# Kernel optimization log

Hardware: AMD Instinct MI355X
Metric: run time of the kernel (lower is better)

The kernel has to match this reference:

```python
import jax, jax.numpy as jnp
import numpy as np

B, N, P, D = 256, 196, 768, 768
FIXED_MASK = 40          # FIXED_MASK_COUNT in the TF source
FIXED_UNMASK = N - FIXED_MASK


def setup_inputs() -> dict:
    key = jax.random.key(0)
    k1, k2, k3, k4, k5 = jax.random.split(key, 5)
    return {
        "patches": jax.random.normal(k1, (B, N, P), jnp.float32),
        "rand_u": jax.random.uniform(k2, (B, N), jnp.float32),
        "W": jax.random.normal(k3, (P, D), jnp.float32) * 0.02,
        "b": jnp.zeros((D,), jnp.float32),
        "pos_table": jax.random.normal(k4, (N, D), jnp.float32) * 0.02,
        "mask_token": jax.random.normal(k5, (1, P), jnp.float32),
    }


def reference(patches, rand_u, W, b, pos_table, mask_token):
    Bsz, Np, _ = patches.shape
    pos = pos_table[None]                                   # [1,N,D]
    patch_emb = jnp.einsum("bnp,pd->bnd", patches, W) + b + pos  # [B,N,D]

    # ---- get_smart_indices ----
    patch_means = jnp.mean(jnp.abs(patches), axis=2)        # [B,N]
    valid_mask = (patch_means > 0).astype(jnp.float32)
    valid_counts = jnp.sum(valid_mask, axis=1)
    max_masks = jnp.ceil(valid_counts * 0.4).astype(jnp.int32)
    valid_image = (valid_counts >= 20) & (max_masks >= FIXED_MASK)  # [B]

    # scores: valid patches in [1000,2000), invalid in [0,10)
    scores = valid_mask * (1000.0 + 1000.0 * rand_u) + (1.0 - valid_mask) * (10.0 * rand_u)
    _, top_idx = jax.lax.top_k(scores, FIXED_MASK)          # first 40 of full top-k sort
    top_idx = top_idx.astype(jnp.int32)
    mask_indices = jnp.where(valid_image[:, None], top_idx, jnp.zeros_like(top_idx))
    mask_counts = jnp.where(valid_image, FIXED_MASK, 0).astype(jnp.int32)

    # complement (ascending order), vectorized stream compaction via sort key
    flag = jnp.zeros((Bsz, Np), jnp.int32).at[jnp.arange(Bsz)[:, None], mask_indices].set(1)
    sort_key = flag * Np + jnp.arange(Np, dtype=jnp.int32)[None]  # unmasked sort first, ascending
    comp = jnp.argsort(sort_key, axis=1)[:, :FIXED_UNMASK].astype(jnp.int32)
    unmask_indices = jnp.where(valid_image[:, None], comp,
                               jnp.arange(FIXED_UNMASK, dtype=jnp.int32)[None])

    # ---- batched gathers ----
    pos_b = jnp.broadcast_to(pos, patch_emb.shape)          # [B,N,D]
    take = lambda x, i: jnp.take_along_axis(x, i[..., None], axis=1)
    unmasked_embeddings = take(patch_emb, unmask_indices)   # [B,156,D]
    unmasked_positions = take(pos_b, unmask_indices)        # [B,156,D]
    masked_positions = take(pos_b, mask_indices)            # [B,40,D]

    mtok = mask_token @ W + b                               # [1,D]
    masked_embeddings = mtok[None] + masked_positions       # [B,40,D]

    # validity masking (counts are 40 for valid images, 0 otherwise)
    seq = jnp.arange(FIXED_MASK, dtype=jnp.int32)[None]
    validity = (seq < mask_counts[:, None]).astype(jnp.float32)[..., None]
    masked_embeddings = masked_embeddings * validity

    return (unmasked_embeddings, masked_embeddings, unmasked_positions,
            mask_indices, unmask_indices)
```

## Files before the change

kernel.cpp:

```cpp
#include <hip/hip_runtime.h>
#include <hip/hip_bf16.h>
#include <stdint.h>

#define BATCH 256
#define NP    196
#define PP    768
#define DD    768
#define FM    40
#define FU    156

#define O_UE 0ull
#define O_ME 30670848ull
#define O_UP 38535168ull
#define O_MI 69206016ull
#define O_UI 69216256ull

typedef __attribute__((ext_vector_type(8))) short short8;
typedef __attribute__((ext_vector_type(4))) float f32x4;

__device__ __forceinline__ unsigned short bf16_rne(float x) {
    unsigned u = __float_as_uint(x);
    u += 0x7FFFu + ((u >> 16) & 1u);
    return (unsigned short)(u >> 16);
}
__device__ __forceinline__ float bf16_f(unsigned short h) {
    return __uint_as_float(((unsigned)h) << 16);
}

__global__ __launch_bounds__(256) void prep_w_kernel(
    const float* __restrict__ W,
    unsigned short* __restrict__ wt_hi,
    unsigned short* __restrict__ wt_lo) {
    const int d  = blockIdx.x * 256 + threadIdx.x;
    const int kt = blockIdx.y;
    alignas(16) unsigned short hi[32];
    alignas(16) unsigned short lo[32];
#pragma unroll
    for (int g = 0; g < 4; ++g) {
#pragma unroll
        for (int j = 0; j < 8; ++j) {
            int k = (j < 4) ? (4 * g + j) : (16 + 4 * g + (j - 4));
            float x = W[(size_t)(kt * 32 + k) * DD + d];
            unsigned short h = bf16_rne(x);
            hi[g * 8 + j] = h;
            lo[g * 8 + j] = bf16_rne(x - bf16_f(h));
        }
    }
    size_t base = ((size_t)kt * DD + d) * 32;
    uint4* dh = (uint4*)(wt_hi + base);
    uint4* dl = (uint4*)(wt_lo + base);
    const uint4* sh = (const uint4*)hi;
    const uint4* sl = (const uint4*)lo;
#pragma unroll
    for (int i = 0; i < 4; ++i) { dh[i] = sh[i]; dl[i] = sl[i]; }
}

__global__ __launch_bounds__(256) void mtok_kernel(
    const float* __restrict__ mask_token,
    const float* __restrict__ W,
    const float* __restrict__ bias,
    float* __restrict__ mtok_out) {
    int d = blockIdx.x * 256 + threadIdx.x;
    if (d >= DD) return;
    float acc = 0.f;
    for (int p = 0; p < PP; ++p) acc += mask_token[p] * W[(size_t)p * DD + d];
    mtok_out[d] = acc + bias[d];
}

__global__ __launch_bounds__(256) void select_kernel(
    const float* __restrict__ patches,
    const float* __restrict__ rand_u,
    float* __restrict__ out,
    int* __restrict__ gidx,
    int* __restrict__ pidx,
    int* __restrict__ midx,
    int* __restrict__ valid_arr) {

    const int b = blockIdx.x;
    const int tid = threadIdx.x;
    __shared__ unsigned long long key[256];
    __shared__ int s_flag[256];
    __shared__ int s_scan[256];
    __shared__ int wsum[4];

    int v = 0;
    if (tid < NP) {
        const float* row = patches + ((size_t)b * NP + tid) * PP;
        for (int p = 0; p < PP; ++p) {
            if (row[p] != 0.0f) { v = 1; break; }
        }
    }
    unsigned long long bal = __ballot(v != 0);
    if ((tid & 63) == 0) wsum[tid >> 6] = __popcll(bal);
    __syncthreads();
    int count = wsum[0] + wsum[1] + wsum[2] + wsum[3];
    bool valid_image = (count >= 20) && (ceilf((float)count * 0.4f) >= 40.0f);

    unsigned long long k = 0ull;
    if (tid < NP) {
        float u = rand_u[(size_t)b * NP + tid];
        float score = v ? (1000.0f + 1000.0f * u) : (10.0f * u);
        k = (((unsigned long long)__float_as_uint(score)) << 32) |
            (unsigned long long)(unsigned)(~tid);
    }
    key[tid] = k;
    __syncthreads();

    for (int kk = 2; kk <= 256; kk <<= 1) {
        for (int j = kk >> 1; j > 0; j >>= 1) {
            int ixj = tid ^ j;
            if (ixj > tid) {
                unsigned long long a = key[tid], c = key[ixj];
                bool desc = ((tid & kk) == 0);
                if (desc ? (a < c) : (a > c)) { key[tid] = c; key[ixj] = a; }
            }
            __syncthreads();
        }
    }

    int m_out = 0;
    if (tid < FM) {
        int idx = (int)(~(unsigned)(key[tid] & 0xFFFFFFFFull));
        m_out = valid_image ? idx : 0;
        midx[b * FM + tid] = m_out;
        out[O_MI + (size_t)b * FM + tid] = (float)m_out;
    }
    s_flag[tid] = 0;
    __syncthreads();
    if (tid < FM) s_flag[m_out] = 1;
    __syncthreads();

    int x = (tid < NP) ? (1 - s_flag[tid]) : 0;
    s_scan[tid] = x;
    __syncthreads();
    for (int off = 1; off < 256; off <<= 1) {
        int t2 = (tid >= off) ? s_scan[tid - off] : 0;
        __syncthreads();
        s_scan[tid] += t2;
        __syncthreads();
    }
    int pos = s_scan[tid] - x;

    if (valid_image) {
        if (tid < NP && !s_flag[tid] && pos < FU) {
            gidx[(size_t)b * FU + pos] = b * NP + tid;
            pidx[(size_t)b * FU + pos] = tid;
            out[O_UI + (size_t)b * FU + pos] = (float)tid;
        }
    } else {
        if (tid < FU) {
            gidx[(size_t)b * FU + tid] = b * NP + tid;
            pidx[(size_t)b * FU + tid] = tid;
            out[O_UI + (size_t)b * FU + tid] = (float)tid;
        }
    }
    if (tid == 0) valid_arr[b] = valid_image ? 1 : 0;
}

__global__ __launch_bounds__(256) void gemm_kernel(
    const float* __restrict__ patches,
    const unsigned short* __restrict__ wt_hi,
    const unsigned short* __restrict__ wt_lo,
    const float* __restrict__ bias,
    const float* __restrict__ pos_table,
    const int* __restrict__ gidx,
    const int* __restrict__ pidx,
    float* __restrict__ out) {

    __shared__ __align__(16) unsigned short lds_hi[128 * 32];
    __shared__ __align__(16) unsigned short lds_lo[128 * 32];

    const int tid = threadIdx.x;
    const int l   = tid & 63;
    const int w   = tid >> 6;
    const int wd  = w >> 1;
    const int wp  = w & 1;
    const int ct  = blockIdx.x;
    const int rt  = blockIdx.y;
    const int l15 = l & 15;
    const int g   = l >> 4;

    int rflat[4];
    const float* prow[4];
    int ppos[4];
#pragma unroll
    for (int ci = 0; ci < 4; ++ci) {
        int r = rt * 128 + wp * 64 + ci * 16 + l15;
        rflat[ci] = r;
        prow[ci] = patches + (size_t)gidx[r] * PP;
        ppos[ci] = pidx[r];
    }

    f32x4 acc[4][4];
    const f32x4 z = {0.f, 0.f, 0.f, 0.f};
#pragma unroll
    for (int mi = 0; mi < 4; ++mi)
#pragma unroll
        for (int ci = 0; ci < 4; ++ci) acc[mi][ci] = z;

    const size_t tile_us0 = (size_t)(ct * 128) * 32;
    uint4* ldsv_hi = (uint4*)lds_hi;
    uint4* ldsv_lo = (uint4*)lds_lo;

    for (int kt = 0; kt < 24; ++kt) {
        short8 phi[4], plo[4];
#pragma unroll
        for (int ci = 0; ci < 4; ++ci) {
            const float* p = prow[ci] + kt * 32 + 4 * g;
            const float4 a  = *(const float4*)p;
            const float4 b2 = *(const float4*)(p + 16);
            float vs[8] = {a.x, a.y, a.z, a.w, b2.x, b2.y, b2.z, b2.w};
            short8 h8, l8;
#pragma unroll
            for (int e = 0; e < 8; ++e) {
                unsigned short h = bf16_rne(vs[e]);
                h8[e] = (short)h;
                l8[e] = (short)bf16_rne(vs[e] - bf16_f(h));
            }
            phi[ci] = h8;
            plo[ci] = l8;
        }

        const uint4* sh = (const uint4*)(wt_hi + (size_t)kt * DD * 32 + tile_us0);
        const uint4* sl = (const uint4*)(wt_lo + (size_t)kt * DD * 32 + tile_us0);
        ldsv_hi[tid]       = sh[tid];
        ldsv_hi[tid + 256] = sh[tid + 256];
        ldsv_lo[tid]       = sl[tid];
        ldsv_lo[tid + 256] = sl[tid + 256];
        __syncthreads();

#pragma unroll
        for (int mi = 0; mi < 4; ++mi) {
            const int rowbase = (wd * 64 + mi * 16 + l15) * 32 + g * 8;
            short8 whi = *(const short8*)(lds_hi + rowbase);
            short8 wlo = *(const short8*)(lds_lo + rowbase);
#pragma unroll
            for (int ci = 0; ci < 4; ++ci) {
                acc[mi][ci] = __builtin_amdgcn_mfma_f32_16x16x32_bf16(
                    whi, phi[ci], acc[mi][ci], 0, 0, 0);
                acc[mi][ci] = __builtin_amdgcn_mfma_f32_16x16x32_bf16(
                    whi, plo[ci], acc[mi][ci], 0, 0, 0);
                acc[mi][ci] = __builtin_amdgcn_mfma_f32_16x16x32_bf16(
                    wlo, phi[ci], acc[mi][ci], 0, 0, 0);
            }
        }
        __syncthreads();
    }

#pragma unroll
    for (int mi = 0; mi < 4; ++mi) {
        const int dc = ct * 128 + wd * 64 + mi * 16 + 4 * g;
        const float4 b4 = *(const float4*)(bias + dc);
#pragma unroll
        for (int ci = 0; ci < 4; ++ci) {
            const float4 p4 = *(const float4*)(pos_table + (size_t)ppos[ci] * DD + dc);
            f32x4 o = acc[mi][ci];
            float4 r;
            r.x = o[0] + b4.x + p4.x;
            r.y = o[1] + b4.y + p4.y;
            r.z = o[2] + b4.z + p4.z;
            r.w = o[3] + b4.w + p4.w;
            size_t ro = (size_t)rflat[ci] * DD + dc;
            *(float4*)(out + O_UE + ro) = r;
            *(float4*)(out + O_UP + ro) = p4;
        }
    }
}

__global__ __launch_bounds__(192) void masked_kernel(
    const float* __restrict__ pos_table,
    const float* __restrict__ mtok,
    const int* __restrict__ midx,
    const int* __restrict__ valid_arr,
    float* __restrict__ out) {
    const int j = blockIdx.x;
    const int b = blockIdx.y;
    const int d = threadIdx.x * 4;
    float4 r = {0.f, 0.f, 0.f, 0.f};
    if (valid_arr[b]) {
        int pi = midx[b * FM + j];
        const float4 m4 = *(const float4*)(mtok + d);
        const float4 p4 = *(const float4*)(pos_table + (size_t)pi * DD + d);
        r.x = m4.x + p4.x; r.y = m4.y + p4.y;
        r.z = m4.z + p4.z; r.w = m4.w + p4.w;
    }
    *(float4*)(out + O_ME + ((size_t)b * FM + j) * DD + d) = r;
}

extern "C" void kernel_launch(void* const* d_in, const int* in_sizes, int n_in,
                              void* d_out, int out_size, void* d_ws, size_t ws_size,
                              hipStream_t stream) {
    const float* patches   = (const float*)d_in[0];
    const float* rand_u    = (const float*)d_in[1];
    const float* W         = (const float*)d_in[2];
    const float* bias      = (const float*)d_in[3];
    const float* pos_table = (const float*)d_in[4];
    const float* mask_tok  = (const float*)d_in[5];
    float* out = (float*)d_out;

    char* ws = (char*)d_ws;
    int*            gidx   = (int*)(ws + 0);
    int*            pidx   = (int*)(ws + 159744);
    int*            midx   = (int*)(ws + 319488);
    int*            valid  = (int*)(ws + 360448);
    float*          mtok   = (float*)(ws + 361472);
    unsigned short* wt_hi  = (unsigned short*)(ws + 364544);
    unsigned short* wt_lo  = (unsigned short*)(ws + 1544192);

    prep_w_kernel<<<dim3(3, 24), dim3(256), 0, stream>>>(W, wt_hi, wt_lo);
    mtok_kernel<<<dim3(3), dim3(256), 0, stream>>>(mask_tok, W, bias, mtok);
    select_kernel<<<dim3(BATCH), dim3(256), 0, stream>>>(patches, rand_u, out,
                                                         gidx, pidx, midx, valid);
    gemm_kernel<<<dim3(6, 312), dim3(256), 0, stream>>>(patches, wt_hi, wt_lo,
                                                        bias, pos_table, gidx,
                                                        pidx, out);
    masked_kernel<<<dim3(FM, BATCH), dim3(192), 0, stream>>>(pos_table, mtok,
                                                             midx, valid, out);
}
```

Before: 667.7 us.

## Double-buffer GEMM with direct-to-LDS loads, pre-split patches, swizzled W

The GEMM now double-buffers the W tile in LDS, filled by global_load_lds, and prefetches the next K-step's B fragments while the current step computes. W is prepacked into a swizzled per-tile layout, and the block index is remapped to group tiles for cache reuse. A new pre-pass splits the gathered patches into bf16 hi/lo parts when the workspace is large enough, taking that conversion out of the GEMM loop. The mask-token matvec is split into partial sums plus a reduction. The patch pre-pass writes and reads an extra ~120MB buffer, which may cost more memory traffic than the conversion work it removes.

```diff
diff --git a/kernel.cpp b/kernel.cpp
--- a/kernel.cpp
+++ b/kernel.cpp
@@ -8,6 +8,7 @@
 #define DD    768
 #define FM    40
 #define FU    156
+#define ROWS  39936
 
 #define O_UE 0ull
 #define O_ME 30670848ull
@@ -27,44 +28,61 @@
     return __uint_as_float(((unsigned)h) << 16);
 }
 
+__device__ __forceinline__ void gl_lds16(const void* gsrc, void* ldst) {
+    __builtin_amdgcn_global_load_lds(
+        (const __attribute__((address_space(1))) unsigned*)gsrc,
+        (__attribute__((address_space(3))) unsigned*)ldst, 16, 0, 0);
+}
+
 __global__ __launch_bounds__(256) void prep_w_kernel(
     const float* __restrict__ W,
-    unsigned short* __restrict__ wt_hi,
-    unsigned short* __restrict__ wt_lo) {
-    const int d  = blockIdx.x * 256 + threadIdx.x;
-    const int kt = blockIdx.y;
-    alignas(16) unsigned short hi[32];
-    alignas(16) unsigned short lo[32];
-#pragma unroll
-    for (int g = 0; g < 4; ++g) {
-#pragma unroll
-        for (int j = 0; j < 8; ++j) {
-            int k = (j < 4) ? (4 * g + j) : (16 + 4 * g + (j - 4));
-            float x = W[(size_t)(kt * 32 + k) * DD + d];
-            unsigned short h = bf16_rne(x);
-            hi[g * 8 + j] = h;
-            lo[g * 8 + j] = bf16_rne(x - bf16_f(h));
-        }
-    }
-    size_t base = ((size_t)kt * DD + d) * 32;
-    uint4* dh = (uint4*)(wt_hi + base);
-    uint4* dl = (uint4*)(wt_lo + base);
-    const uint4* sh = (const uint4*)hi;
-    const uint4* sl = (const uint4*)lo;
-#pragma unroll
-    for (int i = 0; i < 4; ++i) { dh[i] = sh[i]; dl[i] = sl[i]; }
-}
-
-__global__ __launch_bounds__(256) void mtok_kernel(
+    unsigned short* __restrict__ wt) {
+    const int j  = blockIdx.x * 256 + threadIdx.x;
+    const int ct = blockIdx.y;
+    const int kt = blockIdx.z;
+    const int row  = j >> 2;
+    const int slot = j & 3;
+    const int g    = slot ^ ((row >> 1) & 3);
+    const int d    = ct * 128 + row;
+    alignas(16) unsigned short hi[8];
+    alignas(16) unsigned short lo[8];
+#pragma unroll
+    for (int e = 0; e < 8; ++e) {
+        int k32 = (e < 4) ? (4 * g + e) : (12 + 4 * g + e);
+        float x = W[(size_t)(kt * 32 + k32) * DD + d];
+        unsigned short h = bf16_rne(x);
+        hi[e] = h;
+        lo[e] = bf16_rne(x - bf16_f(h));
+    }
+    unsigned short* dst = wt + ((size_t)(kt * 6 + ct) * 1024 + j) * 8;
+    *(uint4*)dst          = *(const uint4*)hi;
+    *(uint4*)(dst + 4096) = *(const uint4*)lo;
+}
+
+__global__ __launch_bounds__(256) void mtok_part_kernel(
     const float* __restrict__ mask_token,
     const float* __restrict__ W,
+    float* __restrict__ part) {
+    const int j = blockIdx.x;
+    const int tid = threadIdx.x;
+#pragma unroll
+    for (int s = 0; s < 3; ++s) {
+        int d = tid + s * 256;
+        float acc = 0.f;
+        for (int p = j * 64; p < j * 64 + 64; ++p)
+            acc += mask_token[p] * W[(size_t)p * DD + d];
+        part[(size_t)j * DD + d] = acc;
+    }
+}
+__global__ __launch_bounds__(256) void mtok_red_kernel(
+    const float* __restrict__ part,
     const float* __restrict__ bias,
     float* __restrict__ mtok_out) {
     int d = blockIdx.x * 256 + threadIdx.x;
-    if (d >= DD) return;
-    float acc = 0.f;
-    for (int p = 0; p < PP; ++p) acc += mask_token[p] * W[(size_t)p * DD + d];
-    mtok_out[d] = acc + bias[d];
+    float acc = bias[d];
+#pragma unroll
+    for (int j = 0; j < 12; ++j) acc += part[(size_t)j * DD + d];
+    mtok_out[d] = acc;
 }
 
 __global__ __launch_bounds__(256) void select_kernel(
@@ -99,7 +117,8 @@
     unsigned long long k = 0ull;
     if (tid < NP) {
         float u = rand_u[(size_t)b * NP + tid];
-        float score = v ? (1000.0f + 1000.0f * u) : (10.0f * u);
+        float score = v ? __fadd_rn(1000.0f, __fmul_rn(1000.0f, u))
+                        : __fmul_rn(10.0f, u);
         k = (((unsigned long long)__float_as_uint(score)) << 32) |
             (unsigned long long)(unsigned)(~tid);
     }
@@ -157,38 +176,104 @@
     if (tid == 0) valid_arr[b] = valid_image ? 1 : 0;
 }
 
+__global__ __launch_bounds__(192) void prep_p_kernel(
+    const float* __restrict__ patches,
+    const int* __restrict__ gidx,
+    char* __restrict__ pat_bf) {
+    const int r = blockIdx.x;
+    const int t = threadIdx.x;
+    const float* src = patches + (size_t)gidx[r] * PP;
+    float4 v4 = *(const float4*)(src + 4 * t);
+    const int kt = t >> 3;
+    const int q  = t & 7;
+    const int g  = q & 3;
+    const int half = q >> 2;
+    float vs[4] = {v4.x, v4.y, v4.z, v4.w};
+    unsigned long long hp = 0, lp = 0;
+#pragma unroll
+    for (int e = 0; e < 4; ++e) {
+        unsigned short h = bf16_rne(vs[e]);
+        unsigned short l = bf16_rne(vs[e] - bf16_f(h));
+        hp |= ((unsigned long long)h) << (16 * e);
+        lp |= ((unsigned long long)l) << (16 * e);
+    }
+    char* dst = pat_bf + (size_t)r * 3072 + kt * 64 + g * 16 + half * 8;
+    *(unsigned long long*)dst          = hp;
+    *(unsigned long long*)(dst + 1536) = lp;
+}
+
+template <int PRE>
+__device__ __forceinline__ void fetchB(int KT, short8 (&BH)[4], short8 (&BL)[4],
+                                       const char* const (&pb)[4],
+                                       const float* const (&prow)[4], int g) {
+    if constexpr (PRE) {
+#pragma unroll
+        for (int ci = 0; ci < 4; ++ci) {
+            const char* p = pb[ci] + KT * 64;
+            BH[ci] = *(const short8*)p;
+            BL[ci] = *(const short8*)(p + 1536);
+        }
+    } else {
+#pragma unroll
+        for (int ci = 0; ci < 4; ++ci) {
+            const float* p = prow[ci] + KT * 32 + 4 * g;
+            const float4 a  = *(const float4*)p;
+            const float4 b2 = *(const float4*)(p + 16);
+            float vs[8] = {a.x, a.y, a.z, a.w, b2.x, b2.y, b2.z, b2.w};
+            short8 h8, l8;
+#pragma unroll
+            for (int e = 0; e < 8; ++e) {
+                unsigned short h = bf16_rne(vs[e]);
+                h8[e] = (short)h;
+                l8[e] = (short)bf16_rne(vs[e] - bf16_f(h));
+            }
+            BH[ci] = h8;
+            BL[ci] = l8;
+        }
+    }
+}
+
+template <int PRE>
 __global__ __launch_bounds__(256) void gemm_kernel(
     const float* __restrict__ patches,
-    const unsigned short* __restrict__ wt_hi,
-    const unsigned short* __restrict__ wt_lo,
+    const char* __restrict__ pat_bf,
+    const unsigned short* __restrict__ wt,
     const float* __restrict__ bias,
     const float* __restrict__ pos_table,
     const int* __restrict__ gidx,
     const int* __restrict__ pidx,
     float* __restrict__ out) {
 
-    __shared__ __align__(16) unsigned short lds_hi[128 * 32];
-    __shared__ __align__(16) unsigned short lds_lo[128 * 32];
+    __shared__ __align__(16) char ldsb[32768];
 
     const int tid = threadIdx.x;
     const int l   = tid & 63;
     const int w   = tid >> 6;
     const int wd  = w >> 1;
     const int wp  = w & 1;
-    const int ct  = blockIdx.x;
-    const int rt  = blockIdx.y;
     const int l15 = l & 15;
     const int g   = l >> 4;
+    const int slot = g ^ ((l15 >> 1) & 3);
+
+    int lin = blockIdx.y * 6 + blockIdx.x;
+    lin = (lin & 7) * 234 + (lin >> 3);
+    const int ct = lin % 6;
+    const int rt = lin / 6;
 
     int rflat[4];
-    const float* prow[4];
     int ppos[4];
+    const char* pb[4]   = {nullptr, nullptr, nullptr, nullptr};
+    const float* prow[4] = {nullptr, nullptr, nullptr, nullptr};
 #pragma unroll
     for (int ci = 0; ci < 4; ++ci) {
         int r = rt * 128 + wp * 64 + ci * 16 + l15;
         rflat[ci] = r;
-        prow[ci] = patches + (size_t)gidx[r] * PP;
         ppos[ci] = pidx[r];
+        if constexpr (PRE) {
+            pb[ci] = pat_bf + (size_t)r * 3072 + g * 16;
+        } else {
+            prow[ci] = patches + (size_t)gidx[r] * PP;
+        }
     }
 
     f32x4 acc[4][4];
@@ -198,54 +283,52 @@
 #pragma unroll
         for (int ci = 0; ci < 4; ++ci) acc[mi][ci] = z;
 
-    const size_t tile_us0 = (size_t)(ct * 128) * 32;
-    uint4* ldsv_hi = (uint4*)lds_hi;
-    uint4* ldsv_lo = (uint4*)lds_lo;
-
-    for (int kt = 0; kt < 24; ++kt) {
-        short8 phi[4], plo[4];
-#pragma unroll
-        for (int ci = 0; ci < 4; ++ci) {
-            const float* p = prow[ci] + kt * 32 + 4 * g;
-            const float4 a  = *(const float4*)p;
-            const float4 b2 = *(const float4*)(p + 16);
-            float vs[8] = {a.x, a.y, a.z, a.w, b2.x, b2.y, b2.z, b2.w};
-            short8 h8, l8;
-#pragma unroll
-            for (int e = 0; e < 8; ++e) {
-                unsigned short h = bf16_rne(vs[e]);
-                h8[e] = (short)h;
-                l8[e] = (short)bf16_rne(vs[e] - bf16_f(h));
-            }
-            phi[ci] = h8;
-            plo[ci] = l8;
-        }
-
-        const uint4* sh = (const uint4*)(wt_hi + (size_t)kt * DD * 32 + tile_us0);
-        const uint4* sl = (const uint4*)(wt_lo + (size_t)kt * DD * 32 + tile_us0);
-        ldsv_hi[tid]       = sh[tid];
-        ldsv_hi[tid + 256] = sh[tid + 256];
-        ldsv_lo[tid]       = sl[tid];
-        ldsv_lo[tid + 256] = sl[tid + 256];
+#define STAGE(BUF, KT)                                                         \
+    {                                                                          \
+        const char* s0 = (const char*)wt + (size_t)((KT)*6 + ct) * 16384;      \
+        _Pragma("unroll")                                                      \
+        for (int c = 0; c < 4; ++c) {                                          \
+            gl_lds16(s0 + ((c * 4 + w) * 64 + l) * 16,                         \
+                     ldsb + (BUF)*16384 + (c * 4 + w) * 1024);                 \
+        }                                                                      \
+    }
+
+#define COMPUTE(BUF, BH, BL)                                                   \
+    _Pragma("unroll")                                                          \
+    for (int mi = 0; mi < 4; ++mi) {                                           \
+        const char* wb = ldsb + (BUF)*16384 +                                  \
+                         (wd * 64 + mi * 16 + l15) * 64 + slot * 16;           \
+        short8 wh = *(const short8*)wb;                                        \
+        short8 wl = *(const short8*)(wb + 8192);                               \
+        _Pragma("unroll")                                                      \
+        for (int ci = 0; ci < 4; ++ci) {                                       \
+            acc[mi][ci] = __builtin_amdgcn_mfma_f32_16x16x32_bf16(             \
+                wh, BH[ci], acc[mi][ci], 0, 0, 0);                             \
+            acc[mi][ci] = __builtin_amdgcn_mfma_f32_16x16x32_bf16(             \
+                wh, BL[ci], acc[mi][ci], 0, 0, 0);                             \
+            acc[mi][ci] = __builtin_amdgcn_mfma_f32_16x16x32_bf16(             \
+                wl, BH[ci], acc[mi][ci], 0, 0, 0);                             \
+        }                                                                      \
+    }
+
+    short8 bhA[4], blA[4], bhB[4], blB[4];
+    fetchB<PRE>(0, bhA, blA, pb, prow, g);
+    STAGE(0, 0);
+
+    for (int kt = 0; kt < 24; kt += 2) {
         __syncthreads();
-
-#pragma unroll
-        for (int mi = 0; mi < 4; ++mi) {
-            const int rowbase = (wd * 64 + mi * 16 + l15) * 32 + g * 8;
-            short8 whi = *(const short8*)(lds_hi + rowbase);
-            short8 wlo = *(const short8*)(lds_lo + rowbase);
-#pragma unroll
-            for (int ci = 0; ci < 4; ++ci) {
-                acc[mi][ci] = __builtin_amdgcn_mfma_f32_16x16x32_bf16(
-                    whi, phi[ci], acc[mi][ci], 0, 0, 0);
-                acc[mi][ci] = __builtin_amdgcn_mfma_f32_16x16x32_bf16(
-                    whi, plo[ci], acc[mi][ci], 0, 0, 0);
-                acc[mi][ci] = __builtin_amdgcn_mfma_f32_16x16x32_bf16(
-                    wlo, phi[ci], acc[mi][ci], 0, 0, 0);
-            }
-        }
+        STAGE(1, kt + 1);
+        fetchB<PRE>(kt + 1, bhB, blB, pb, prow, g);
+        COMPUTE(0, bhA, blA);
         __syncthreads();
-    }
+        if (kt + 2 < 24) {
+            STAGE(0, kt + 2);
+            fetchB<PRE>(kt + 2, bhA, blA, pb, prow, g);
+        }
+        COMPUTE(1, bhB, blB);
+    }
+#undef STAGE
+#undef COMPUTE
 
 #pragma unroll
     for (int mi = 0; mi < 4; ++mi) {
@@ -304,16 +387,26 @@
     int*            midx   = (int*)(ws + 319488);
     int*            valid  = (int*)(ws + 360448);
     float*          mtok   = (float*)(ws + 361472);
-    unsigned short* wt_hi  = (unsigned short*)(ws + 364544);
-    unsigned short* wt_lo  = (unsigned short*)(ws + 1544192);
-
-    prep_w_kernel<<<dim3(3, 24), dim3(256), 0, stream>>>(W, wt_hi, wt_lo);
-    mtok_kernel<<<dim3(3), dim3(256), 0, stream>>>(mask_tok, W, bias, mtok);
+    float*          mpart  = (float*)(ws + 364544);
+    unsigned short* wt     = (unsigned short*)(ws + 401408);
+    char*           pat_bf = ws + 2760704;
+
+    const size_t NEEDED = 2760704ull + 122683392ull;
+    const bool pre = (ws_size >= NEEDED);
+
+    prep_w_kernel<<<dim3(2, 6, 24), dim3(256), 0, stream>>>(W, wt);
+    mtok_part_kernel<<<dim3(12), dim3(256), 0, stream>>>(mask_tok, W, mpart);
+    mtok_red_kernel<<<dim3(3), dim3(256), 0, stream>>>(mpart, bias, mtok);
     select_kernel<<<dim3(BATCH), dim3(256), 0, stream>>>(patches, rand_u, out,
                                                          gidx, pidx, midx, valid);
-    gemm_kernel<<<dim3(6, 312), dim3(256), 0, stream>>>(patches, wt_hi, wt_lo,
-                                                        bias, pos_table, gidx,
-                                                        pidx, out);
+    if (pre) {
+        prep_p_kernel<<<dim3(ROWS), dim3(192), 0, stream>>>(patches, gidx, pat_bf);
+        gemm_kernel<1><<<dim3(6, 312), dim3(256), 0, stream>>>(
+            patches, pat_bf, wt, bias, pos_table, gidx, pidx, out);
+    } else {
+        gemm_kernel<0><<<dim3(6, 312), dim3(256), 0, stream>>>(
+            patches, pat_bf, wt, bias, pos_table, gidx, pidx, out);
+    }
     masked_kernel<<<dim3(FM, BATCH), dim3(192), 0, stream>>>(pos_table, mtok,
                                                              midx, valid, out);
 }
```

Result: slower. 707.2 us (+5.9%).
